# Kernel optimization log

Measured on AMD Instinct MI355X. Metric: run time of the kernel, lower is better.

## Reference

```python
import jax, jax.numpy as jnp
import numpy as np

N, K, IN_C, OUT_C = 100000, 128, 128, 128


def setup_inputs() -> dict:
    key = jax.random.key(0)
    k1, k2, k3 = jax.random.split(key, 3)
    x = jax.random.normal(k1, (N, IN_C), dtype=jnp.float32)
    U = jax.random.normal(k2, (N, K), dtype=jnp.float32)
    coeffs = jax.random.normal(k3, (OUT_C, K, IN_C), dtype=jnp.float32)
    return {"x": x, "U": U, "coeffs": coeffs}


def reference(x, U, coeffs):
    # U.T @ x : (K, in_channels)
    spec = jnp.einsum('nk,ni->ki', U, x)
    # coeffs * spec, summed over in_channels : (out_channels, K)
    mixed = jnp.einsum('oki,ki->ok', coeffs, spec)
    # U @ mixed : (out_channels, N)
    out = jnp.einsum('nk,ok->on', U, mixed)
    # softmax over N (dim=-1), then transpose -> (N, out_channels)
    return jax.nn.softmax(out, axis=-1).T
```

## Files before the change

### kernel.cpp

```cpp
#include <hip/hip_runtime.h>
#include <math.h>

#define N_PTS 100000
#define KDIM 128
#define CDIM 128
#define TILE_N 64
#define NB1 ((N_PTS + TILE_N - 1) / TILE_N)

typedef short s16x8 __attribute__((ext_vector_type(8)));
typedef float f32x4 __attribute__((ext_vector_type(4)));

static __device__ __forceinline__ unsigned short f2bf(float f) {
    unsigned int u = __float_as_uint(f);
    unsigned int r = (u + 0x7FFFu + ((u >> 16) & 1u)) >> 16;
    return (unsigned short)r;
}
static __device__ __forceinline__ float bf2f(unsigned short h) {
    return __uint_as_float(((unsigned int)h) << 16);
}

static __device__ __forceinline__ void split_trunc(float v, unsigned short& hi, unsigned short& lo) {
    unsigned int u = __float_as_uint(v);
    unsigned int uh = u & 0xFFFF0000u;
    float lf = v - __uint_as_float(uh);
    hi = (unsigned short)(u >> 16);
    lo = (unsigned short)(__float_as_uint(lf) >> 16);
}

__global__ __launch_bounds__(512, 4) void kA(const float* __restrict__ U,
                                             const float* __restrict__ x,
                                             float* __restrict__ partials,
                                             int chunk) {
    __shared__ unsigned short Hs[2][8192];
    __shared__ unsigned short Ls[2][8192];
    const int tid = threadIdx.x;
    const int b = blockIdx.x;
    const int n_begin = b * chunk;
    const int n_end = min(N_PTS, n_begin + chunk);
    const int lane = tid & 63;
    const int w = tid >> 6;
    const int mtb = (w & 3) * 2;
    const int ntb = (w >> 2) * 4;
    const int quad = lane >> 4;
    const int nl = lane & 15;

    const int arr = tid >> 8;
    const float* __restrict__ src = arr ? x : U;
    const int c4 = (tid & 31) * 4;
    const int rq = (tid >> 5) & 7;
    const int Tt = c4 >> 4;
    const int ssub = rq >> 2;
    const int R = rq & 3;

    f32x4 acc[2][4];
#pragma unroll
    for (int mi = 0; mi < 2; ++mi)
#pragma unroll
        for (int ni = 0; ni < 4; ++ni) acc[mi][ni] = (f32x4)(0.0f);

    for (int n0 = n_begin; n0 < n_end; n0 += 64) {
        float4 v[8];
#pragma unroll
        for (int jj = 0; jj < 8; ++jj) {
            int gn = n0 + rq * 8 + jj;
            v[jj] = (gn < n_end) ? *(const float4*)&src[(size_t)gn * 128 + c4]
                                 : make_float4(0, 0, 0, 0);
        }
#pragma unroll
        for (int cc = 0; cc < 4; ++cc) {
            s16x8 hh, ll;
#pragma unroll
            for (int jj = 0; jj < 8; ++jj) {
                unsigned short h, l;
                split_trunc(((const float*)&v[jj])[cc], h, l);
                hh[jj] = (short)h;
                ll[jj] = (short)l;
            }
            const int c = c4 + cc;
            const int g = Tt * 64 + R * 16 + ((c & 15) ^ Tt);
            const int dst = ssub * 4096 + g * 8;
            *(s16x8*)&Hs[arr][dst] = hh;
            *(s16x8*)&Ls[arr][dst] = ll;
        }
        __syncthreads();

#pragma unroll
        for (int sub = 0; sub < 2; ++sub) {
            const int base = sub * 4096;
            s16x8 ah[2], al[2];
#pragma unroll
            for (int mi = 0; mi < 2; ++mi) {
                const int T = mtb + mi;
                const int off = base + (T * 64 + quad * 16 + (nl ^ T)) * 8;
                ah[mi] = *(s16x8*)&Hs[0][off];
                al[mi] = *(s16x8*)&Ls[0][off];
            }
#pragma unroll
            for (int ni = 0; ni < 4; ++ni) {
                const int T2 = ntb + ni;
                const int off = base + (T2 * 64 + quad * 16 + (nl ^ T2)) * 8;
                s16x8 bh = *(s16x8*)&Hs[1][off];
                s16x8 bl = *(s16x8*)&Ls[1][off];
#pragma unroll
                for (int mi = 0; mi < 2; ++mi) {
                    acc[mi][ni] = __builtin_amdgcn_mfma_f32_16x16x32_bf16(ah[mi], bh, acc[mi][ni], 0, 0, 0);
                    acc[mi][ni] = __builtin_amdgcn_mfma_f32_16x16x32_bf16(al[mi], bh, acc[mi][ni], 0, 0, 0);
                    acc[mi][ni] = __builtin_amdgcn_mfma_f32_16x16x32_bf16(ah[mi], bl, acc[mi][ni], 0, 0, 0);
                }
            }
        }
        __syncthreads();
    }

    float* p = partials + (size_t)b * 16384;
#pragma unroll
    for (int mi = 0; mi < 2; ++mi) {
#pragma unroll
        for (int reg = 0; reg < 4; ++reg) {
            int k = (mtb + mi) * 16 + quad * 4 + reg;
#pragma unroll
            for (int ni = 0; ni < 4; ++ni) {
                int i = (ntb + ni) * 16 + nl;
                p[k * 128 + i] = acc[mi][ni][reg];
            }
        }
    }
}

__global__ __launch_bounds__(256) void kA2a(const float* __restrict__ partials,
                                            float* __restrict__ partial2, int nA) {
    const int jc = blockIdx.x >> 3;
    const int s = blockIdx.x & 7;
    const int j = jc * 256 + threadIdx.x;
    const int per = (nA + 7) >> 3;
    int b = s * per;
    const int be = min(b + per, nA);
    float a0 = 0.0f, a1 = 0.0f, a2 = 0.0f, a3 = 0.0f;
    for (; b + 4 <= be; b += 4) {
        a0 += partials[(size_t)(b + 0) * 16384 + j];
        a1 += partials[(size_t)(b + 1) * 16384 + j];
        a2 += partials[(size_t)(b + 2) * 16384 + j];
        a3 += partials[(size_t)(b + 3) * 16384 + j];
    }
    for (; b < be; ++b) a0 += partials[(size_t)b * 16384 + j];
    partial2[(size_t)s * 16384 + j] = (a0 + a1) + (a2 + a3);
}

__global__ __launch_bounds__(256) void kB(const float* __restrict__ coeffs,
                                          const float* __restrict__ partial2,
                                          unsigned short* __restrict__ afrag_hi,
                                          unsigned short* __restrict__ afrag_lo) {
    int wave = (blockIdx.x * 256 + threadIdx.x) >> 6;
    int lane = threadIdx.x & 63;
    int o = wave >> 7;
    int k = wave & 127;
    const int j = k * 128 + lane * 2;
    float2 p0 = *(const float2*)&partial2[j];
    float2 p1 = *(const float2*)&partial2[16384 + j];
    float2 p2 = *(const float2*)&partial2[2 * 16384 + j];
    float2 p3 = *(const float2*)&partial2[3 * 16384 + j];
    float2 p4 = *(const float2*)&partial2[4 * 16384 + j];
    float2 p5 = *(const float2*)&partial2[5 * 16384 + j];
    float2 p6 = *(const float2*)&partial2[6 * 16384 + j];
    float2 p7 = *(const float2*)&partial2[7 * 16384 + j];
    float sx = ((p0.x + p1.x) + (p2.x + p3.x)) + ((p4.x + p5.x) + (p6.x + p7.x));
    float sy = ((p0.y + p1.y) + (p2.y + p3.y)) + ((p4.y + p5.y) + (p6.y + p7.y));
    float2 c2 = *(const float2*)&coeffs[((size_t)o * 128 + k) * 128 + lane * 2];
    float v = c2.x * sx + c2.y * sy;
#pragma unroll
    for (int s = 32; s >= 1; s >>= 1) v += __shfl_xor(v, s);
    if (lane == 0) {
        unsigned short hi = f2bf(v);
        unsigned short lo = f2bf(v - bf2f(hi));
        int idx = ((o >> 4) * 4 + (k >> 5)) * 512 + (((k >> 3) & 3) * 16 + (o & 15)) * 8 + (k & 7);
        afrag_hi[idx] = hi;
        afrag_lo[idx] = lo;
    }
}

__global__ __launch_bounds__(512) void kC1(const float* __restrict__ U,
                                           const unsigned short* __restrict__ afrag_hi,
                                           const unsigned short* __restrict__ afrag_lo,
                                           float* __restrict__ out,
                                           float* __restrict__ m_part,
                                           float* __restrict__ l_part) {
    __shared__ unsigned short Bh[8192];
    __shared__ unsigned short Bl[8192];
    const int tid = threadIdx.x;
    const int b = blockIdx.x;
    const int n0 = b * TILE_N;
    const int lane = tid & 63;
    const int w = tid >> 6;
    const int quad = lane >> 4;
    const int nl = lane & 15;

    {
        const int sn = tid & 63;
        const int k8b = tid >> 6;
        const int gn = n0 + sn;
#pragma unroll
        for (int r = 0; r < 2; ++r) {
            const int k0 = (k8b + r * 8) * 8;
            float4 f0 = make_float4(0, 0, 0, 0), f1 = make_float4(0, 0, 0, 0);
            if (gn < N_PTS) {
                f0 = *(const float4*)&U[(size_t)gn * 128 + k0];
                f1 = *(const float4*)&U[(size_t)gn * 128 + k0 + 4];
            }
            float vv[8] = {f0.x, f0.y, f0.z, f0.w, f1.x, f1.y, f1.z, f1.w};
            s16x8 hh, ll;
#pragma unroll
            for (int jj = 0; jj < 8; ++jj) {
                unsigned short h, l;
                split_trunc(vv[jj], h, l);
                hh[jj] = (short)h;
                ll[jj] = (short)l;
            }
            const int T = (k0 >> 5) * 4 + (sn >> 4);
            const int g = T * 64 + ((k0 >> 3) & 3) * 16 + ((sn & 15) ^ (T & 3));
            *(s16x8*)&Bh[g * 8] = hh;
            *(s16x8*)&Bl[g * 8] = ll;
        }
    }

    s16x8 Ah[4], Al[4];
#pragma unroll
    for (int kc = 0; kc < 4; ++kc) {
        size_t aoff = (size_t)(w * 4 + kc) * 512 + lane * 8;
        Ah[kc] = *(const s16x8*)(afrag_hi + aoff);
        Al[kc] = *(const s16x8*)(afrag_lo + aoff);
    }

    __syncthreads();

    f32x4 acc[4];
#pragma unroll
    for (int nt = 0; nt < 4; ++nt) acc[nt] = (f32x4)(0.0f);

#pragma unroll
    for (int kc = 0; kc < 4; ++kc) {
#pragma unroll
        for (int nt = 0; nt < 4; ++nt) {
            const int T = kc * 4 + nt;
            const int g = T * 64 + quad * 16 + (nl ^ (T & 3));
            s16x8 bh = *(s16x8*)&Bh[g * 8];
            s16x8 bl = *(s16x8*)&Bl[g * 8];
            acc[nt] = __builtin_amdgcn_mfma_f32_16x16x32_bf16(Ah[kc], bh, acc[nt], 0, 0, 0);
            acc[nt] = __builtin_amdgcn_mfma_f32_16x16x32_bf16(Al[kc], bh, acc[nt], 0, 0, 0);
            acc[nt] = __builtin_amdgcn_mfma_f32_16x16x32_bf16(Ah[kc], bl, acc[nt], 0, 0, 0);
        }
    }

#pragma unroll
    for (int nt = 0; nt < 4; ++nt) {
        if (n0 + nt * 16 + nl >= N_PTS) {
#pragma unroll
            for (int reg = 0; reg < 4; ++reg) acc[nt][reg] = -3.4e38f;
        }
    }

    float mb[4];
#pragma unroll
    for (int reg = 0; reg < 4; ++reg)
        mb[reg] = fmaxf(fmaxf(acc[0][reg], acc[1][reg]), fmaxf(acc[2][reg], acc[3][reg]));
#pragma unroll
    for (int s = 1; s < 16; s <<= 1) {
#pragma unroll
        for (int reg = 0; reg < 4; ++reg) mb[reg] = fmaxf(mb[reg], __shfl_xor(mb[reg], s));
    }

#pragma unroll
    for (int nt = 0; nt < 4; ++nt) {
#pragma unroll
        for (int reg = 0; reg < 4; ++reg) acc[nt][reg] = __expf(acc[nt][reg] - mb[reg]);
        int gn = n0 + nt * 16 + nl;
        if (gn < N_PTS)
            *(f32x4*)&out[(size_t)gn * 128 + w * 16 + quad * 4] = acc[nt];
    }

    float ls[4];
#pragma unroll
    for (int reg = 0; reg < 4; ++reg)
        ls[reg] = ((acc[0][reg] + acc[1][reg]) + (acc[2][reg] + acc[3][reg]));
#pragma unroll
    for (int s = 1; s < 16; s <<= 1) {
#pragma unroll
        for (int reg = 0; reg < 4; ++reg) ls[reg] += __shfl_xor(ls[reg], s);
    }

    if (nl == 0) {
#pragma unroll
        for (int reg = 0; reg < 4; ++reg) {
            int o = w * 16 + quad * 4 + reg;
            m_part[(size_t)o * NB1 + b] = mb[reg];
            l_part[(size_t)o * NB1 + b] = ls[reg];
        }
    }
}

__global__ __launch_bounds__(256) void kC2(const float* __restrict__ m_part,
                                           const float* __restrict__ l_part,
                                           float* __restrict__ scale) {
    const int o = blockIdx.x;
    const int tid = threadIdx.x;
    const float* __restrict__ mp = m_part + (size_t)o * NB1;
    const float* __restrict__ lp = l_part + (size_t)o * NB1;
    __shared__ float sm[256];
    float m = -3.4e38f;
    for (int b = tid; b < NB1; b += 256) m = fmaxf(m, mp[b]);
    sm[tid] = m;
    __syncthreads();
    for (int s = 128; s >= 1; s >>= 1) {
        if (tid < s) sm[tid] = fmaxf(sm[tid], sm[tid + s]);
        __syncthreads();
    }
    m = sm[0];
    __syncthreads();
    float l = 0.0f;
    for (int b = tid; b < NB1; b += 256)
        l += lp[b] * __expf(mp[b] - m);
    sm[tid] = l;
    __syncthreads();
    for (int s = 128; s >= 1; s >>= 1) {
        if (tid < s) sm[tid] += sm[tid + s];
        __syncthreads();
    }
    l = sm[0];
    float inv = 1.0f / l;
    for (int b = tid; b < NB1; b += 256)
        scale[(size_t)o * NB1 + b] = __expf(mp[b] - m) * inv;
}

__global__ __launch_bounds__(256) void kC3(float* __restrict__ out,
                                           const float* __restrict__ scale) {
    const int b = blockIdx.x;
    const int tid = threadIdx.x;
    __shared__ float sc[128];
    if (tid < 128) sc[tid] = scale[(size_t)tid * NB1 + b];
    __syncthreads();
    const int n0 = b * TILE_N;
#pragma unroll
    for (int r = 0; r < 8; ++r) {
        int idx = (r * 256 + tid) * 4;
        int n = idx >> 7;
        int o = idx & 127;
        int gn = n0 + n;
        if (gn < N_PTS) {
            float4 v = *(float4*)&out[(size_t)gn * 128 + o];
            v.x *= sc[o];
            v.y *= sc[o + 1];
            v.z *= sc[o + 2];
            v.w *= sc[o + 3];
            *(float4*)&out[(size_t)gn * 128 + o] = v;
        }
    }
}

extern "C" void kernel_launch(void* const* d_in, const int* in_sizes, int n_in,
                              void* d_out, int out_size, void* d_ws, size_t ws_size,
                              hipStream_t stream) {
    const float* x = (const float*)d_in[0];
    const float* U = (const float*)d_in[1];
    const float* coeffs = (const float*)d_in[2];
    float* out = (float*)d_out;

    float* f = (float*)d_ws;
    float* spec = f;
    unsigned short* afrag_hi = (unsigned short*)(f + 16384);
    unsigned short* afrag_lo = (unsigned short*)(f + 16384 + 8192);
    float* m_part = f + 16384 + 16384;
    float* l_part = m_part + (size_t)128 * NB1;
    float* scale = l_part + (size_t)128 * NB1;
    float* partial2 = scale + (size_t)128 * NB1;
    float* partialsA = partial2 + 8 * 16384;
    (void)spec;

    size_t fixed_bytes = ((size_t)(16384 * 2) + (size_t)NB1 * 128 * 3 + (size_t)8 * 16384) * 4;
    int nA = 512;
    if (ws_size > fixed_bytes) {
        size_t avail = (ws_size - fixed_bytes) / 65536;
        if ((size_t)nA > avail) nA = (int)avail;
    } else {
        nA = 1;
    }
    if (nA < 1) nA = 1;
    int chunk = (N_PTS + nA - 1) / nA;

    kA<<<nA, 512, 0, stream>>>(U, x, partialsA, chunk);
    kA2a<<<512, 256, 0, stream>>>(partialsA, partial2, nA);
    kB<<<4096, 256, 0, stream>>>(coeffs, partial2, afrag_hi, afrag_lo);
    kC1<<<NB1, 512, 0, stream>>>(U, afrag_hi, afrag_lo, out, m_part, l_part);
    kC2<<<128, 256, 0, stream>>>(m_part, l_part, scale);
    kC3<<<NB1, 256, 0, stream>>>(out, scale);
}
```

Measured before the change: 212.0 us.

## Double-buffer kA LDS tiles and prefetch next rows during MFMA

Restructures the U^T x reduction kernel so each step handles 32 rows using a double-buffered shared-memory tile. The next tile's global loads are issued before the MFMA work and converted into the buffer afterwards, leaving one barrier per iteration. Each thread now loads scalar floats from both U and x instead of float4 from one array, and the XOR swizzle is removed. The chunk size is rounded to a multiple of 32 and the grid size is recomputed. The goal is to overlap memory latency with compute, at the cost of narrower loads and possible LDS bank conflicts.

```diff
diff --git a/kernel.cpp b/kernel.cpp
--- a/kernel.cpp
+++ b/kernel.cpp
@@ -31,8 +31,7 @@
                                              const float* __restrict__ x,
                                              float* __restrict__ partials,
                                              int chunk) {
-    __shared__ unsigned short Hs[2][8192];
-    __shared__ unsigned short Ls[2][8192];
+    __shared__ unsigned short SB[2][4][4096];
     const int tid = threadIdx.x;
     const int b = blockIdx.x;
     const int n_begin = b * chunk;
@@ -44,13 +43,9 @@
     const int quad = lane >> 4;
     const int nl = lane & 15;
 
-    const int arr = tid >> 8;
-    const float* __restrict__ src = arr ? x : U;
-    const int c4 = (tid & 31) * 4;
-    const int rq = (tid >> 5) & 7;
-    const int Tt = c4 >> 4;
-    const int ssub = rq >> 2;
-    const int R = rq & 3;
+    const int sc = tid & 127;
+    const int rq = tid >> 7;
+    const int sgran = (sc >> 4) * 64 + rq * 16 + (sc & 15);
 
     f32x4 acc[2][4];
 #pragma unroll
@@ -58,49 +53,61 @@
 #pragma unroll
         for (int ni = 0; ni < 4; ++ni) acc[mi][ni] = (f32x4)(0.0f);
 
-    for (int n0 = n_begin; n0 < n_end; n0 += 64) {
-        float4 v[8];
+    float uv[8], xv[8];
+
+    {
+        const int r0 = n_begin + rq * 8;
 #pragma unroll
         for (int jj = 0; jj < 8; ++jj) {
-            int gn = n0 + rq * 8 + jj;
-            v[jj] = (gn < n_end) ? *(const float4*)&src[(size_t)gn * 128 + c4]
-                                 : make_float4(0, 0, 0, 0);
-        }
-#pragma unroll
-        for (int cc = 0; cc < 4; ++cc) {
-            s16x8 hh, ll;
+            int gn = r0 + jj;
+            bool ok = (gn < n_end);
+            uv[jj] = ok ? U[(size_t)gn * 128 + sc] : 0.0f;
+            xv[jj] = ok ? x[(size_t)gn * 128 + sc] : 0.0f;
+        }
+        s16x8 uh, ul, xh, xl;
+#pragma unroll
+        for (int jj = 0; jj < 8; ++jj) {
+            unsigned short h, l;
+            split_trunc(uv[jj], h, l);
+            uh[jj] = (short)h; ul[jj] = (short)l;
+            split_trunc(xv[jj], h, l);
+            xh[jj] = (short)h; xl[jj] = (short)l;
+        }
+        *(s16x8*)&SB[0][0][sgran * 8] = uh;
+        *(s16x8*)&SB[0][1][sgran * 8] = ul;
+        *(s16x8*)&SB[0][2][sgran * 8] = xh;
+        *(s16x8*)&SB[0][3][sgran * 8] = xl;
+    }
+    __syncthreads();
+
+    const int nIters = (n_end - n_begin + 31) >> 5;
+    for (int it = 0; it < nIters; ++it) {
+        const bool more = (it + 1 < nIters);
+        if (more) {
+            const int r0 = n_begin + (it + 1) * 32 + rq * 8;
 #pragma unroll
             for (int jj = 0; jj < 8; ++jj) {
-                unsigned short h, l;
-                split_trunc(((const float*)&v[jj])[cc], h, l);
-                hh[jj] = (short)h;
-                ll[jj] = (short)l;
-            }
-            const int c = c4 + cc;
-            const int g = Tt * 64 + R * 16 + ((c & 15) ^ Tt);
-            const int dst = ssub * 4096 + g * 8;
-            *(s16x8*)&Hs[arr][dst] = hh;
-            *(s16x8*)&Ls[arr][dst] = ll;
-        }
-        __syncthreads();
-
-#pragma unroll
-        for (int sub = 0; sub < 2; ++sub) {
-            const int base = sub * 4096;
+                int gn = r0 + jj;
+                bool ok = (gn < n_end);
+                uv[jj] = ok ? U[(size_t)gn * 128 + sc] : 0.0f;
+                xv[jj] = ok ? x[(size_t)gn * 128 + sc] : 0.0f;
+            }
+        }
+
+        {
+            const int buf = it & 1;
             s16x8 ah[2], al[2];
 #pragma unroll
             for (int mi = 0; mi < 2; ++mi) {
-                const int T = mtb + mi;
-                const int off = base + (T * 64 + quad * 16 + (nl ^ T)) * 8;
-                ah[mi] = *(s16x8*)&Hs[0][off];
-                al[mi] = *(s16x8*)&Ls[0][off];
+                const int off = ((mtb + mi) * 64 + lane) * 8;
+                ah[mi] = *(s16x8*)&SB[buf][0][off];
+                al[mi] = *(s16x8*)&SB[buf][1][off];
             }
 #pragma unroll
             for (int ni = 0; ni < 4; ++ni) {
-                const int T2 = ntb + ni;
-                const int off = base + (T2 * 64 + quad * 16 + (nl ^ T2)) * 8;
-                s16x8 bh = *(s16x8*)&Hs[1][off];
-                s16x8 bl = *(s16x8*)&Ls[1][off];
+                const int off = ((ntb + ni) * 64 + lane) * 8;
+                s16x8 bh = *(s16x8*)&SB[buf][2][off];
+                s16x8 bl = *(s16x8*)&SB[buf][3][off];
 #pragma unroll
                 for (int mi = 0; mi < 2; ++mi) {
                     acc[mi][ni] = __builtin_amdgcn_mfma_f32_16x16x32_bf16(ah[mi], bh, acc[mi][ni], 0, 0, 0);
@@ -108,6 +115,23 @@
                     acc[mi][ni] = __builtin_amdgcn_mfma_f32_16x16x32_bf16(ah[mi], bl, acc[mi][ni], 0, 0, 0);
                 }
             }
+        }
+
+        if (more) {
+            const int buf = (it + 1) & 1;
+            s16x8 uh, ul, xh, xl;
+#pragma unroll
+            for (int jj = 0; jj < 8; ++jj) {
+                unsigned short h, l;
+                split_trunc(uv[jj], h, l);
+                uh[jj] = (short)h; ul[jj] = (short)l;
+                split_trunc(xv[jj], h, l);
+                xh[jj] = (short)h; xl[jj] = (short)l;
+            }
+            *(s16x8*)&SB[buf][0][sgran * 8] = uh;
+            *(s16x8*)&SB[buf][1][sgran * 8] = ul;
+            *(s16x8*)&SB[buf][2][sgran * 8] = xh;
+            *(s16x8*)&SB[buf][3][sgran * 8] = xl;
         }
         __syncthreads();
     }
@@ -383,10 +407,11 @@
         nA = 1;
     }
     if (nA < 1) nA = 1;
-    int chunk = (N_PTS + nA - 1) / nA;
-
-    kA<<<nA, 512, 0, stream>>>(U, x, partialsA, chunk);
-    kA2a<<<512, 256, 0, stream>>>(partialsA, partial2, nA);
+    int chunk = (((N_PTS + nA - 1) / nA) + 31) & ~31;
+    int nB = (N_PTS + chunk - 1) / chunk;
+
+    kA<<<nB, 512, 0, stream>>>(U, x, partialsA, chunk);
+    kA2a<<<512, 256, 0, stream>>>(partialsA, partial2, nB);
     kB<<<4096, 256, 0, stream>>>(coeffs, partial2, afrag_hi, afrag_lo);
     kC1<<<NB1, 512, 0, stream>>>(U, afrag_hi, afrag_lo, out, m_part, l_part);
     kC2<<<128, 256, 0, stream>>>(m_part, l_part, scale);
```

Result: faster. 204.9 us (-3.4%).
